# Kernel tuning notes

Hardware: AMD Instinct MI355X
Metric: run time of the kernel (lower is better)

The kernel has to match this reference:

```python
import jax, jax.numpy as jnp
import numpy as np

NUM_GROUPS = 32
EPS = 1e-6


def group_norm(x, scale, bias):
    # x: [b, c, l]
    b, c, l = x.shape
    xg = x.reshape(b, NUM_GROUPS, (c // NUM_GROUPS) * l)
    mean = jnp.mean(xg, axis=2, keepdims=True)
    var = jnp.var(xg, axis=2, keepdims=True)
    xn = ((xg - mean) * jax.lax.rsqrt(var + EPS)).reshape(b, c, l)
    return xn * scale[None, :, None] + bias[None, :, None]


def conv1x1(x, w, b):
    # pointwise conv: w [out_c, in_c], x [b, in_c, l]
    return jnp.einsum('oc,bcl->bol', w, x) + b[None, :, None]


def setup_inputs() -> dict:
    key = jax.random.key(0)
    ks = jax.random.split(key, 11)
    b, c, l = 4, 512, 4096
    s = 1.0 / np.sqrt(c)
    return {
        'x': jax.random.normal(ks[0], (b, c, l), jnp.float32),
        'gn_scale': jnp.ones((c,), jnp.float32),
        'gn_bias': jnp.zeros((c,), jnp.float32),
        'wq': jax.random.normal(ks[1], (c, c), jnp.float32) * s,
        'bq': jnp.zeros((c,), jnp.float32),
        'wk': jax.random.normal(ks[2], (c, c), jnp.float32) * s,
        'bk': jnp.zeros((c,), jnp.float32),
        'wv': jax.random.normal(ks[3], (c, c), jnp.float32) * s,
        'bv': jnp.zeros((c,), jnp.float32),
        'wp': jax.random.normal(ks[4], (c, c), jnp.float32) * s,
        'bp': jnp.zeros((c,), jnp.float32),
    }


def reference(x, gn_scale, gn_bias, wq, bq, wk, bk, wv, bv, wp, bp):
    h_ = group_norm(x, gn_scale, gn_bias)
    q = conv1x1(h_, wq, bq)  # [b, c, l]
    k = conv1x1(h_, wk, bk)
    v = conv1x1(h_, wv, bv)
    c = q.shape[1]
    # scores w[b,i,j] = sum_c q[b,c,i] k[b,c,j] * c^-0.5, softmax over j
    w = jnp.einsum('bci,bcj->bij', q, k) * (c ** -0.5)
    w = jax.nn.softmax(w, axis=2)
    # out[b,c,i] = sum_j w[b,i,j] v[b,c,j]
    h_ = jnp.einsum('bij,bcj->bci', w, v)
    h_ = conv1x1(h_, wp, bp)
    return x + h_
```

## Files before the change

kernel.cpp:

```cpp
#include <hip/hip_runtime.h>
#include <math.h>

#define BB 4
#define CC 512
#define LL 4096
#define NG 32
#define CPG 16
#define EPSV 1e-6f

typedef short s16x8 __attribute__((ext_vector_type(8)));
typedef __bf16 bf8v __attribute__((ext_vector_type(8)));
typedef float f32x4 __attribute__((ext_vector_type(4)));
typedef float f32x16 __attribute__((ext_vector_type(16)));
typedef int i32x4 __attribute__((ext_vector_type(4)));
typedef int i32x8 __attribute__((ext_vector_type(8)));
typedef unsigned short u16;
typedef unsigned char u8;

typedef const __attribute__((address_space(1))) void g1_void;
typedef __attribute__((address_space(3))) void l3_void;

#define ASM_SBAR() asm volatile("s_barrier" ::: "memory")
#define ASM_WAITV(N) asm volatile("s_waitcnt vmcnt(" #N ")" ::: "memory")

static __device__ __forceinline__ float bf2f(u16 h) {
    unsigned int u = ((unsigned int)h) << 16;
    union { unsigned int u; float f; } c; c.u = u; return c.f;
}
static __device__ __forceinline__ u16 f2bf(float f) {
    union { float f; unsigned int u; } c; c.f = f;
    unsigned int lsb = (c.u >> 16) & 1u;
    c.u += 0x7fffu + lsb;
    return (u16)(c.u >> 16);
}
static __device__ __forceinline__ u8 f2fp8(float f) {
    int v = __builtin_amdgcn_cvt_pk_fp8_f32(f, f, 0, false);
    return (u8)(v & 0xff);
}
static __device__ __forceinline__ bf8v ld_bf8(const u16* p) {
    return *reinterpret_cast<const bf8v*>(p);
}
static __device__ __forceinline__ i32x8 ld32(const u8* plo, const u8* phi) {
    i32x4 lo = *reinterpret_cast<const i32x4*>(plo);
    i32x4 hi = *reinterpret_cast<const i32x4*>(phi);
    return __builtin_shufflevector(lo, hi, 0, 1, 2, 3, 4, 5, 6, 7);
}
#define MFMA_SC(a, b, c) \
    __builtin_amdgcn_mfma_scale_f32_32x32x64_f8f6f4(a, b, c, 0, 0, 0, 0x7f, 0, 0x7f)

static __device__ __forceinline__ void gload16(const u16* g, u16* l) {
    __builtin_amdgcn_global_load_lds((g1_void*)g, (l3_void*)l, 16, 0, 0);
}
static __device__ __forceinline__ void gload16b(const u8* g, u8* l) {
    __builtin_amdgcn_global_load_lds((g1_void*)g, (l3_void*)l, 16, 0, 0);
}

__global__ __launch_bounds__(256) void wconv_kernel(const float* __restrict__ w0,
                                                    const float* __restrict__ w1,
                                                    const float* __restrict__ w2,
                                                    const float* __restrict__ w3,
                                                    u16* __restrict__ wbf) {
    int i = blockIdx.x * 256 + threadIdx.x;
    int wsel = blockIdx.y;
    const float* src = (wsel == 0) ? w0 : (wsel == 1) ? w1 : (wsel == 2) ? w2 : w3;
    float4 v = reinterpret_cast<const float4*>(src)[i];
    ushort4 o;
    o.x = f2bf(v.x); o.y = f2bf(v.y); o.z = f2bf(v.z); o.w = f2bf(v.w);
    reinterpret_cast<ushort4*>(wbf + (size_t)wsel * CC * CC)[i] = o;
}

__global__ __launch_bounds__(256) void biascat_kernel(const float* __restrict__ bq,
                                                      const float* __restrict__ bk,
                                                      const float* __restrict__ bv,
                                                      float* __restrict__ bcat,
                                                      float* __restrict__ rowsum) {
    int i = blockIdx.x * 256 + threadIdx.x;
    if (i < 3 * CC) {
        float v = (i < CC) ? bq[i] : (i < 2 * CC ? bk[i - CC] : bv[i - 2 * CC]);
        bcat[i] = v;
    }
    if (i < BB * LL) rowsum[i] = 0.f;
}

__global__ __launch_bounds__(256) void gn_stats_kernel(const float* __restrict__ x,
                                                       float2* __restrict__ stats) {
    int g = blockIdx.x, b = blockIdx.y, t = threadIdx.x;
    const float4* xp = reinterpret_cast<const float4*>(x + ((size_t)b * CC + (size_t)g * CPG) * LL);
    float s = 0.f, ss = 0.f;
    for (int it = 0; it < 64; ++it) {
        float4 v = xp[it * 256 + t];
        s += v.x + v.y + v.z + v.w;
        ss += v.x * v.x + v.y * v.y + v.z * v.z + v.w * v.w;
    }
    #pragma unroll
    for (int off = 32; off; off >>= 1) { s += __shfl_xor(s, off, 64); ss += __shfl_xor(ss, off, 64); }
    __shared__ float rs[4], rss[4];
    int wave = t >> 6, lane = t & 63;
    if (lane == 0) { rs[wave] = s; rss[wave] = ss; }
    __syncthreads();
    if (t == 0) {
        float S = rs[0] + rs[1] + rs[2] + rs[3];
        float SS = rss[0] + rss[1] + rss[2] + rss[3];
        float mean = S * (1.f / 65536.f);
        float var = SS * (1.f / 65536.f) - mean * mean;
        var = fmaxf(var, 0.f);
        stats[b * NG + g] = make_float2(mean, rsqrtf(var + EPSV));
    }
}

__global__ __launch_bounds__(256) void gn_norm_t_kernel(const float* __restrict__ x,
                                                        const float2* __restrict__ stats,
                                                        const float* __restrict__ gsc,
                                                        const float* __restrict__ gbi,
                                                        u16* __restrict__ hT) {
    int lt = blockIdx.x, ct = blockIdx.y, b = blockIdx.z;
    __shared__ u16 tile[64][72];
    int t = threadIdx.x;
    int cl0 = t >> 4, c4 = (t & 15) * 4;
    #pragma unroll
    for (int p = 0; p < 4; ++p) {
        int cl = p * 16 + cl0;
        int cg = ct * 64 + cl;
        float2 st = stats[b * NG + (cg >> 4)];
        float sc = gsc[cg] * st.y;
        float bi = gbi[cg];
        float4 v = *reinterpret_cast<const float4*>(x + ((size_t)b * CC + cg) * LL + lt * 64 + c4);
        tile[cl][c4 + 0] = f2bf((v.x - st.x) * sc + bi);
        tile[cl][c4 + 1] = f2bf((v.y - st.x) * sc + bi);
        tile[cl][c4 + 2] = f2bf((v.z - st.x) * sc + bi);
        tile[cl][c4 + 3] = f2bf((v.w - st.x) * sc + bi);
    }
    __syncthreads();
    int r = t >> 3, c8 = (t & 7) * 8;
    #pragma unroll
    for (int p = 0; p < 2; ++p) {
        int ll = p * 32 + r;
        s16x8 ov;
        #pragma unroll
        for (int j = 0; j < 8; ++j) ov[j] = (short)tile[c8 + j][ll];
        u16* hp = hT + ((size_t)b * LL + lt * 64 + ll) * CC + ct * 64 + c8;
        *reinterpret_cast<s16x8*>(hp) = ov;
    }
}

template <int MODE>
__global__ __launch_bounds__(256) void gemm_kernel(const u16* __restrict__ A, size_t asb, int lda,
                                                   const u16* __restrict__ B, size_t bsb, int ldb,
                                                   const float* __restrict__ bias,
                                                   u8* __restrict__ Oq, u8* __restrict__ Ok,
                                                   u8* __restrict__ Ov, size_t osb,
                                                   const float* __restrict__ xres,
                                                   float* __restrict__ fout, int K) {
    __shared__ u16 pool[24576];
    u8* pool8 = (u8*)pool;
    int mt = blockIdx.x, nt = blockIdx.y, b = blockIdx.z;
    int t = threadIdx.x;
    int wave = t >> 6, lane = t & 63;
    int wm = (wave >> 1) * 64, wn = (wave & 1) * 64;
    int l15 = lane & 15, quad = lane >> 4;
    f32x4 acc[4][4] = {};
    const u16* Ab = A + (size_t)b * asb + (size_t)mt * 128 * lda;
    const u16* Bb = B + (size_t)b * bsb + (size_t)nt * 128 * ldb;
    int swzg = ((lane & 3) ^ ((lane >> 2) & 3) ^ ((lane >> 4) & 3)) * 8;
    int row0 = wave * 16 + (lane >> 2);
    int row1 = 64 + row0;
    const u16* Ap0 = Ab + (size_t)row0 * lda + swzg;
    const u16* Ap1 = Ab + (size_t)row1 * lda + swzg;
    const u16* Bp0 = Bb + (size_t)row0 * ldb + swzg;
    const u16* Bp1 = Bb + (size_t)row1 * ldb + swzg;
    int wo = wave * 512;
    int swzf = (l15 & 3) ^ (l15 >> 2);
    int aoff = (wm + l15) * 32 + ((quad ^ swzf) * 8);
    int boff = (wn + l15) * 32 + ((quad ^ swzf) * 8);
    const int iters = K >> 5;
    gload16(Ap0, pool + wo);                gload16(Ap1, pool + 2048 + wo);
    gload16(Bp0, pool + 12288 + wo);        gload16(Bp1, pool + 12288 + 2048 + wo);
    gload16(Ap0 + 32, pool + 4096 + wo);    gload16(Ap1 + 32, pool + 4096 + 2048 + wo);
    gload16(Bp0 + 32, pool + 16384 + wo);   gload16(Bp1 + 32, pool + 16384 + 2048 + wo);
    int bs = 0;
    for (int i = 0; i < iters; ++i) {
        if (i + 1 < iters) { ASM_WAITV(4); } else { ASM_WAITV(0); }
        ASM_SBAR();
        const u16* As = pool + bs;
        const u16* Bs = pool + 12288 + bs;
        bf8v af[4], bfr[4];
        #pragma unroll
        for (int ii = 0; ii < 4; ++ii)
            af[ii] = ld_bf8(&As[aoff + ii * 512]);
        #pragma unroll
        for (int j = 0; j < 4; ++j)
            bfr[j] = ld_bf8(&Bs[boff + j * 512]);
        if (i + 2 < iters) {
            int kk = (i + 2) * 32;
            int nb = bs + 8192; if (nb >= 12288) nb -= 12288;
            u16* as = pool + nb; u16* bsp = pool + 12288 + nb;
            gload16(Ap0 + kk, as + wo);        gload16(Ap1 + kk, as + 2048 + wo);
            gload16(Bp0 + kk, bsp + wo);       gload16(Bp1 + kk, bsp + 2048 + wo);
        }
        __builtin_amdgcn_s_setprio(1);
        #pragma unroll
        for (int ii = 0; ii < 4; ++ii)
            #pragma unroll
            for (int j = 0; j < 4; ++j)
                acc[ii][j] = __builtin_amdgcn_mfma_f32_16x16x32_bf16(af[ii], bfr[j], acc[ii][j], 0, 0, 0);
        __builtin_amdgcn_s_setprio(0);
        bs += 4096; if (bs >= 12288) bs -= 12288;
    }
    if (MODE == 0) {
        int nt_sel = nt >> 2, ntl = nt & 3;
        if (nt_sel == 2) {
            __syncthreads();
            #pragma unroll
            for (int j = 0; j < 4; ++j) {
                float bv = bias[nt * 128 + wn + j * 16 + l15];
                #pragma unroll
                for (int i = 0; i < 4; ++i) {
                    int col = wn + j * 16 + l15;
                    int row = wm + i * 16 + quad * 4;
                    unsigned int w = __builtin_amdgcn_cvt_pk_fp8_f32(acc[i][j][0] + bv, acc[i][j][1] + bv, 0, false);
                    w = __builtin_amdgcn_cvt_pk_fp8_f32(acc[i][j][2] + bv, acc[i][j][3] + bv, w, true);
                    *reinterpret_cast<unsigned int*>(&pool8[col * 144 + row]) = w;
                }
            }
            __syncthreads();
            u8* Ob = Ov + (size_t)b * osb + (size_t)(ntl * 128) * LL + mt * 128;
            #pragma unroll
            for (int it = 0; it < 4; ++it) {
                int idx = it * 256 + t;
                int row = idx >> 3, ch = (idx & 7) * 16;
                *reinterpret_cast<float4*>(Ob + (size_t)row * LL + ch) =
                    *reinterpret_cast<const float4*>(&pool8[row * 144 + ch]);
            }
        } else {
            u8* Oc = (nt_sel == 0 ? Oq : Ok) + (size_t)b * osb
                     + (size_t)(mt * 128) * CC + ntl * 128 + wn + l15;
            #pragma unroll
            for (int j = 0; j < 4; ++j) {
                float bv = bias[nt * 128 + wn + j * 16 + l15];
                #pragma unroll
                for (int i = 0; i < 4; ++i)
                    #pragma unroll
                    for (int r = 0; r < 4; ++r) {
                        int row = wm + i * 16 + quad * 4 + r;
                        Oc[(size_t)row * CC + j * 16] = f2fp8(acc[i][j][r] + bv);
                    }
            }
        }
    } else {
        __syncthreads();
        #pragma unroll
        for (int j = 0; j < 4; ++j) {
            float bv = bias[nt * 128 + wn + j * 16 + l15];
            #pragma unroll
            for (int i = 0; i < 4; ++i)
                #pragma unroll
                for (int r = 0; r < 4; ++r) {
                    int row = wm + i * 16 + quad * 4 + r;
                    int col = wn + j * 16 + l15;
                    pool[col * 136 + row] = f2bf(acc[i][j][r] + bv);
                }
        }
        __syncthreads();
        const float* xb = xres + ((size_t)b * CC + nt * 128) * LL + mt * 128;
        float* ob = fout + ((size_t)b * CC + nt * 128) * LL + mt * 128;
        #pragma unroll
        for (int it = 0; it < 16; ++it) {
            int idx = it * 256 + t;
            int cl = idx >> 5, ch = (idx & 31) * 4;
            short4 pv = *reinterpret_cast<const short4*>(&pool[cl * 136 + ch]);
            float4 xv = *reinterpret_cast<const float4*>(xb + (size_t)cl * LL + ch);
            float4 ov;
            ov.x = xv.x + bf2f((u16)pv.x);
            ov.y = xv.y + bf2f((u16)pv.y);
            ov.z = xv.z + bf2f((u16)pv.z);
            ov.w = xv.w + bf2f((u16)pv.w);
            *reinterpret_cast<float4*>(ob + (size_t)cl * LL + ch) = ov;
        }
    }
}

template <int MODE>
__global__ __launch_bounds__(256) void gemm8_kernel(const u8* __restrict__ A, size_t asb, int lda,
                                                    const u8* __restrict__ B, size_t bsb, int ldb,
                                                    float scale,
                                                    u8* __restrict__ Out8, u16* __restrict__ OutH,
                                                    size_t osb, int Nout, int K,
                                                    float* __restrict__ rsum) {
    __shared__ u8 pool8[49152];
    int mt = blockIdx.x, nt = blockIdx.y, b = blockIdx.z;
    int t = threadIdx.x;
    int wave = t >> 6, lane = t & 63;
    int wm = (wave >> 1) * 64, wn = (wave & 1) * 64;
    int l15 = lane & 15, quad = lane >> 4;
    int l31 = lane & 31, hsel = lane >> 5;
    f32x4 acc16[4][4] = {};
    f32x16 accm[2][2] = {};
    int R = wave * 32 + (lane >> 1);
    int c16 = ((lane & 1) ^ (R & 1) ^ ((R >> 2) & 1)) * 16;
    const u8* Ap = A + (size_t)b * asb + (size_t)(mt * 128 + R) * lda + c16;
    const u8* Bp = B + (size_t)b * bsb + (size_t)(nt * 128 + R) * ldb + c16;
    int wo = wave * 1024;
    int p = (l15 & 1) ^ ((l15 >> 2) & 1);
    int fo = (((quad >> 1) ^ p) * 16) + (quad & 1) * 8;
    int abase = (wm + l15) * 32 + fo;
    int bbase = (wn + l15) * 32 + fo;
    int ra = wm + l31;
    int rb = wn + l31;
    int sa = (ra & 1) ^ ((ra >> 2) & 1);
    int sb = (rb & 1) ^ ((rb >> 2) & 1);
    int a_lo = hsel * 4096 + ra * 32 + sa * 16;
    int a_hi = hsel * 4096 + ra * 32 + 16 - sa * 16;
    int b_lo = hsel * 4096 + rb * 32 + sb * 16;
    int b_hi = hsel * 4096 + rb * 32 + 16 - sb * 16;
    const int iters = K >> 6;
    #define STG(ii, bsv) do { size_t kk = (size_t)(ii) * 64;               \
        gload16b(Ap + kk,      pool8 + (bsv) + wo);                        \
        gload16b(Ap + kk + 32, pool8 + (bsv) + 4096 + wo);                 \
        gload16b(Bp + kk,      pool8 + 24576 + (bsv) + wo);                \
        gload16b(Bp + kk + 32, pool8 + 24576 + (bsv) + 4096 + wo); } while (0)
    STG(0, 0);
    STG(1, 8192);
    int bs = 0;
    for (int i = 0; i < iters; ++i) {
        if (i + 1 < iters) { ASM_WAITV(4); } else { ASM_WAITV(0); }
        ASM_SBAR();
        const u8* As = pool8 + bs;
        const u8* Bs = pool8 + 24576 + bs;
        if (MODE == 1) {
            long af0[4], bf0[4], af1[4], bf1[4];
            #pragma unroll
            for (int ii = 0; ii < 4; ++ii) {
                af0[ii] = *reinterpret_cast<const long*>(As + abase + ii * 512);
                af1[ii] = *reinterpret_cast<const long*>(As + 4096 + abase + ii * 512);
            }
            #pragma unroll
            for (int j = 0; j < 4; ++j) {
                bf0[j] = *reinterpret_cast<const long*>(Bs + bbase + j * 512);
                bf1[j] = *reinterpret_cast<const long*>(Bs + 4096 + bbase + j * 512);
            }
            if (i + 2 < iters) {
                int nb = bs + 16384; if (nb >= 24576) nb -= 24576;
                STG(i + 2, nb);
            }
            __builtin_amdgcn_s_setprio(1);
            #pragma unroll
            for (int ii = 0; ii < 4; ++ii)
                #pragma unroll
                for (int j = 0; j < 4; ++j)
                    acc16[ii][j] = __builtin_amdgcn_mfma_f32_16x16x32_fp8_fp8(af0[ii], bf0[j], acc16[ii][j], 0, 0, 0);
            #pragma unroll
            for (int ii = 0; ii < 4; ++ii)
                #pragma unroll
                for (int j = 0; j < 4; ++j)
                    acc16[ii][j] = __builtin_amdgcn_mfma_f32_16x16x32_fp8_fp8(af1[ii], bf1[j], acc16[ii][j], 0, 0, 0);
            __builtin_amdgcn_s_setprio(0);
        } else {
            i32x8 a0 = ld32(As + a_lo, As + a_hi);
            i32x8 a1 = ld32(As + 1024 + a_lo, As + 1024 + a_hi);
            i32x8 b0 = ld32(Bs + b_lo, Bs + b_hi);
            i32x8 b1 = ld32(Bs + 1024 + b_lo, Bs + 1024 + b_hi);
            if (i + 2 < iters) {
                int nb = bs + 16384; if (nb >= 24576) nb -= 24576;
                STG(i + 2, nb);
            }
            __builtin_amdgcn_s_setprio(1);
            accm[0][0] = MFMA_SC(a0, b0, accm[0][0]);
            accm[0][1] = MFMA_SC(a0, b1, accm[0][1]);
            accm[1][0] = MFMA_SC(a1, b0, accm[1][0]);
            accm[1][1] = MFMA_SC(a1, b1, accm[1][1]);
            __builtin_amdgcn_s_setprio(0);
        }
        bs += 8192; if (bs >= 24576) bs -= 24576;
    }
    #undef STG
    if (MODE == 1) {
        u8* Ob = Out8 + (size_t)b * osb + (size_t)(mt * 128) * Nout + nt * 128 + wn + l15;
        #pragma unroll
        for (int i = 0; i < 4; ++i) {
            #pragma unroll
            for (int r = 0; r < 4; ++r) {
                int row = wm + i * 16 + quad * 4 + r;
                u8* rp = Ob + (size_t)row * Nout;
                float part = 0.f;
                #pragma unroll
                for (int j = 0; j < 4; ++j) {
                    float v = __expf(acc16[i][j][r] * scale - 3.0f);
                    part += v;
                    rp[j * 16] = f2fp8(v);
                }
                part += __shfl_xor(part, 1, 64);
                part += __shfl_xor(part, 2, 64);
                part += __shfl_xor(part, 4, 64);
                part += __shfl_xor(part, 8, 64);
                if (l15 == 0)
                    atomicAdd(rsum + (size_t)b * LL + mt * 128 + row, part);
            }
        }
    } else {
        __syncthreads();
        u16* poolh = (u16*)pool8;
        const float* rbase2 = rsum + (size_t)b * LL + mt * 128;
        #pragma unroll
        for (int i = 0; i < 2; ++i)
            #pragma unroll
            for (int rg = 0; rg < 4; ++rg) {
                int row0 = wm + i * 32 + 8 * rg + 4 * hsel;
                float4 rv = *reinterpret_cast<const float4*>(rbase2 + row0);
                float iv[4] = {1.f / rv.x, 1.f / rv.y, 1.f / rv.z, 1.f / rv.w};
                #pragma unroll
                for (int rr = 0; rr < 4; ++rr) {
                    int reg = rg * 4 + rr;
                    int row = row0 + rr;
                    poolh[row * 136 + wn + l31]      = f2bf(accm[i][0][reg] * iv[rr]);
                    poolh[row * 136 + wn + 32 + l31] = f2bf(accm[i][1][reg] * iv[rr]);
                }
            }
        __syncthreads();
        u16* Ob = OutH + (size_t)b * osb + (size_t)(mt * 128) * Nout + nt * 128;
        #pragma unroll
        for (int it = 0; it < 8; ++it) {
            int idx = it * 256 + t;
            int row = idx >> 4, ch = (idx & 15) * 8;
            s16x8 val = *reinterpret_cast<const s16x8*>(&poolh[row * 136 + ch]);
            *reinterpret_cast<s16x8*>(Ob + (size_t)row * Nout + ch) = val;
        }
    }
}

extern "C" void kernel_launch(void* const* d_in, const int* in_sizes, int n_in,
                              void* d_out, int out_size, void* d_ws, size_t ws_size,
                              hipStream_t stream) {
    const float* x   = (const float*)d_in[0];
    const float* gsc = (const float*)d_in[1];
    const float* gbi = (const float*)d_in[2];
    const float* wq  = (const float*)d_in[3];
    const float* bq  = (const float*)d_in[4];
    const float* wk  = (const float*)d_in[5];
    const float* bk  = (const float*)d_in[6];
    const float* wv  = (const float*)d_in[7];
    const float* bv  = (const float*)d_in[8];
    const float* wp  = (const float*)d_in[9];
    const float* bp  = (const float*)d_in[10];
    float* out = (float*)d_out;

    char* ws = (char*)d_ws;
    const size_t SZ   = (size_t)BB * LL * CC * 2;
    const size_t QSZ  = (size_t)BB * LL * CC;
    const size_t WQSZ = (size_t)4 * CC * CC * 2;
    const size_t RSZ  = (size_t)BB * LL * 4;
    u16* bufA = (u16*)(ws);
    u8*  q8   = (u8*)(ws + SZ);
    u8*  k8   = (u8*)(ws + SZ + QSZ);
    u8*  v8   = (u8*)(ws + SZ + 2 * QSZ);
    u16* wbf  = (u16*)(ws + SZ + 3 * QSZ);
    float2* stats = (float2*)(ws + SZ + 3 * QSZ + WQSZ);
    float* bcat   = (float*)(ws + SZ + 3 * QSZ + WQSZ + 4096);
    float* rowsum = (float*)(ws + SZ + 3 * QSZ + WQSZ + 4096 + 8192);
    u8* S8 = (u8*)(ws + SZ + 3 * QSZ + WQSZ + 4096 + 8192 + RSZ);
    const float scale = 0.044194173824159216f;
    const size_t BLC = (size_t)LL * CC;

    wconv_kernel<<<dim3(256, 4), 256, 0, stream>>>(wq, wk, wv, wp, wbf);
    biascat_kernel<<<dim3(64), 256, 0, stream>>>(bq, bk, bv, bcat, rowsum);
    gn_stats_kernel<<<dim3(NG, BB), 256, 0, stream>>>(x, stats);
    gn_norm_t_kernel<<<dim3(64, 8, BB), 256, 0, stream>>>(x, stats, gsc, gbi, bufA);
    gemm_kernel<0><<<dim3(32, 12, BB), 256, 0, stream>>>(bufA, BLC, CC, wbf, 0, CC, bcat,
                                                         q8, k8, v8, BLC, nullptr, nullptr, CC);
    gemm8_kernel<1><<<dim3(32, 32, BB), 256, 0, stream>>>(q8, BLC, CC, k8, BLC, CC, scale,
                                                          S8, nullptr, (size_t)LL * LL, LL, CC, rowsum);
    gemm8_kernel<2><<<dim3(32, 4, BB), 256, 0, stream>>>(S8, (size_t)LL * LL, LL, v8, BLC, LL, 1.f,
                                                         nullptr, bufA, BLC, CC, LL, rowsum);
    gemm_kernel<3><<<dim3(32, 4, BB), 256, 0, stream>>>(bufA, BLC, CC, wbf + 3 * CC * CC, 0, CC,
                                                        bp, nullptr, nullptr, nullptr, 0, x, out, CC);
}
```

Before: 299.9 us.

## Split MODE 1 fp8 score GEMM into 4-stage, 32-wide K pipeline

Separates the MODE 1 (QK^T score) path from the MODE 2 path. MODE 1 now loads a 32-element K slice per iteration into a 4-deep ring of LDS buffers, keeping three stages in flight instead of two 64-wide stages. Its LDS footprint drops to 32 KB, which may allow more resident blocks per CU, and the deeper prefetch aims to hide global load latency. The trade-off is twice as many barriers and loop iterations, with fewer MFMAs between each sync.

```diff
diff --git a/kernel.cpp b/kernel.cpp
--- a/kernel.cpp
+++ b/kernel.cpp
@@ -286,7 +286,7 @@
                                                     u8* __restrict__ Out8, u16* __restrict__ OutH,
                                                     size_t osb, int Nout, int K,
                                                     float* __restrict__ rsum) {
-    __shared__ u8 pool8[49152];
+    __shared__ u8 pool8[MODE == 1 ? 32768 : 49152];
     int mt = blockIdx.x, nt = blockIdx.y, b = blockIdx.z;
     int t = threadIdx.x;
     int wave = t >> 6, lane = t & 63;
@@ -312,68 +312,37 @@
     int a_hi = hsel * 4096 + ra * 32 + 16 - sa * 16;
     int b_lo = hsel * 4096 + rb * 32 + sb * 16;
     int b_hi = hsel * 4096 + rb * 32 + 16 - sb * 16;
-    const int iters = K >> 6;
-    #define STG(ii, bsv) do { size_t kk = (size_t)(ii) * 64;               \
-        gload16b(Ap + kk,      pool8 + (bsv) + wo);                        \
-        gload16b(Ap + kk + 32, pool8 + (bsv) + 4096 + wo);                 \
-        gload16b(Bp + kk,      pool8 + 24576 + (bsv) + wo);                \
-        gload16b(Bp + kk + 32, pool8 + 24576 + (bsv) + 4096 + wo); } while (0)
-    STG(0, 0);
-    STG(1, 8192);
-    int bs = 0;
-    for (int i = 0; i < iters; ++i) {
-        if (i + 1 < iters) { ASM_WAITV(4); } else { ASM_WAITV(0); }
-        ASM_SBAR();
-        const u8* As = pool8 + bs;
-        const u8* Bs = pool8 + 24576 + bs;
-        if (MODE == 1) {
-            long af0[4], bf0[4], af1[4], bf1[4];
-            #pragma unroll
-            for (int ii = 0; ii < 4; ++ii) {
-                af0[ii] = *reinterpret_cast<const long*>(As + abase + ii * 512);
-                af1[ii] = *reinterpret_cast<const long*>(As + 4096 + abase + ii * 512);
-            }
-            #pragma unroll
-            for (int j = 0; j < 4; ++j) {
-                bf0[j] = *reinterpret_cast<const long*>(Bs + bbase + j * 512);
-                bf1[j] = *reinterpret_cast<const long*>(Bs + 4096 + bbase + j * 512);
-            }
-            if (i + 2 < iters) {
-                int nb = bs + 16384; if (nb >= 24576) nb -= 24576;
-                STG(i + 2, nb);
-            }
+    if (MODE == 1) {
+        const int iters = K >> 5;
+        #define STG1(ii) do { size_t kk = (size_t)(ii) * 32; int bb = ((ii) & 3) * 4096; \
+            gload16b(Ap + kk, pool8 + bb + wo);                                          \
+            gload16b(Bp + kk, pool8 + 16384 + bb + wo); } while (0)
+        STG1(0); STG1(1); STG1(2);
+        for (int i = 0; i < iters; ++i) {
+            if (i + 2 < iters) { ASM_WAITV(4); }
+            else if (i + 1 < iters) { ASM_WAITV(2); }
+            else { ASM_WAITV(0); }
+            ASM_SBAR();
+            int bb = (i & 3) * 4096;
+            const u8* As = pool8 + bb;
+            const u8* Bs = pool8 + 16384 + bb;
+            long af[4], bf[4];
+            #pragma unroll
+            for (int ii = 0; ii < 4; ++ii)
+                af[ii] = *reinterpret_cast<const long*>(As + abase + ii * 512);
+            #pragma unroll
+            for (int j = 0; j < 4; ++j)
+                bf[j] = *reinterpret_cast<const long*>(Bs + bbase + j * 512);
+            if (i + 3 < iters) STG1(i + 3);
             __builtin_amdgcn_s_setprio(1);
             #pragma unroll
             for (int ii = 0; ii < 4; ++ii)
                 #pragma unroll
                 for (int j = 0; j < 4; ++j)
-                    acc16[ii][j] = __builtin_amdgcn_mfma_f32_16x16x32_fp8_fp8(af0[ii], bf0[j], acc16[ii][j], 0, 0, 0);
-            #pragma unroll
-            for (int ii = 0; ii < 4; ++ii)
-                #pragma unroll
-                for (int j = 0; j < 4; ++j)
-                    acc16[ii][j] = __builtin_amdgcn_mfma_f32_16x16x32_fp8_fp8(af1[ii], bf1[j], acc16[ii][j], 0, 0, 0);
+                    acc16[ii][j] = __builtin_amdgcn_mfma_f32_16x16x32_fp8_fp8(af[ii], bf[j], acc16[ii][j], 0, 0, 0);
             __builtin_amdgcn_s_setprio(0);
-        } else {
-            i32x8 a0 = ld32(As + a_lo, As + a_hi);
-            i32x8 a1 = ld32(As + 1024 + a_lo, As + 1024 + a_hi);
-            i32x8 b0 = ld32(Bs + b_lo, Bs + b_hi);
-            i32x8 b1 = ld32(Bs + 1024 + b_lo, Bs + 1024 + b_hi);
-            if (i + 2 < iters) {
-                int nb = bs + 16384; if (nb >= 24576) nb -= 24576;
-                STG(i + 2, nb);
-            }
-            __builtin_amdgcn_s_setprio(1);
-            accm[0][0] = MFMA_SC(a0, b0, accm[0][0]);
-            accm[0][1] = MFMA_SC(a0, b1, accm[0][1]);
-            accm[1][0] = MFMA_SC(a1, b0, accm[1][0]);
-            accm[1][1] = MFMA_SC(a1, b1, accm[1][1]);
-            __builtin_amdgcn_s_setprio(0);
-        }
-        bs += 8192; if (bs >= 24576) bs -= 24576;
-    }
-    #undef STG
-    if (MODE == 1) {
+        }
+        #undef STG1
         u8* Ob = Out8 + (size_t)b * osb + (size_t)(mt * 128) * Nout + nt * 128 + wn + l15;
         #pragma unroll
         for (int i = 0; i < 4; ++i) {
@@ -397,6 +366,37 @@
             }
         }
     } else {
+        const int iters = K >> 6;
+        #define STG2(ii, bsv) do { size_t kk = (size_t)(ii) * 64;              \
+            gload16b(Ap + kk,      pool8 + (bsv) + wo);                        \
+            gload16b(Ap + kk + 32, pool8 + (bsv) + 4096 + wo);                 \
+            gload16b(Bp + kk,      pool8 + 24576 + (bsv) + wo);                \
+            gload16b(Bp + kk + 32, pool8 + 24576 + (bsv) + 4096 + wo); } while (0)
+        STG2(0, 0);
+        STG2(1, 8192);
+        int bs = 0;
+        for (int i = 0; i < iters; ++i) {
+            if (i + 1 < iters) { ASM_WAITV(4); } else { ASM_WAITV(0); }
+            ASM_SBAR();
+            const u8* As = pool8 + bs;
+            const u8* Bs = pool8 + 24576 + bs;
+            i32x8 a0 = ld32(As + a_lo, As + a_hi);
+            i32x8 a1 = ld32(As + 1024 + a_lo, As + 1024 + a_hi);
+            i32x8 b0 = ld32(Bs + b_lo, Bs + b_hi);
+            i32x8 b1 = ld32(Bs + 1024 + b_lo, Bs + 1024 + b_hi);
+            if (i + 2 < iters) {
+                int nb = bs + 16384; if (nb >= 24576) nb -= 24576;
+                STG2(i + 2, nb);
+            }
+            __builtin_amdgcn_s_setprio(1);
+            accm[0][0] = MFMA_SC(a0, b0, accm[0][0]);
+            accm[0][1] = MFMA_SC(a0, b1, accm[0][1]);
+            accm[1][0] = MFMA_SC(a1, b0, accm[1][0]);
+            accm[1][1] = MFMA_SC(a1, b1, accm[1][1]);
+            __builtin_amdgcn_s_setprio(0);
+            bs += 8192; if (bs >= 24576) bs -= 24576;
+        }
+        #undef STG2
         __syncthreads();
         u16* poolh = (u16*)pool8;
         const float* rbase2 = rsum + (size_t)b * LL + mt * 128;
```

After: 311.6 us. 1.04x slower.

## Halve PV GEMM M-tile to 64 rows and fold bias setup into weight conversion

Applied to the files above, without the earlier changes.

The attention-times-V GEMM (MODE 2) now uses 64-row M tiles instead of 128, doubling its grid from 512 to 1024 blocks. Each wave computes a 32x64 output with two scaled fp8 MFMAs per K step, and the LDS footprint for that mode shrinks. The aim is to fill the 256 CUs better, since the old grid left many idle during a long K=4096 reduction. The trade is that each V tile is loaded twice as often. Separately, the bias concat and rowsum zeroing move into the weight-conversion kernel, removing one launch.

```diff
diff --git a/kernel.cpp b/kernel.cpp
--- a/kernel.cpp
+++ b/kernel.cpp
@@ -59,7 +59,12 @@
                                                     const float* __restrict__ w1,
                                                     const float* __restrict__ w2,
                                                     const float* __restrict__ w3,
-                                                    u16* __restrict__ wbf) {
+                                                    u16* __restrict__ wbf,
+                                                    const float* __restrict__ bq,
+                                                    const float* __restrict__ bk,
+                                                    const float* __restrict__ bv,
+                                                    float* __restrict__ bcat,
+                                                    float* __restrict__ rowsum) {
     int i = blockIdx.x * 256 + threadIdx.x;
     int wsel = blockIdx.y;
     const float* src = (wsel == 0) ? w0 : (wsel == 1) ? w1 : (wsel == 2) ? w2 : w3;
@@ -67,19 +72,11 @@
     ushort4 o;
     o.x = f2bf(v.x); o.y = f2bf(v.y); o.z = f2bf(v.z); o.w = f2bf(v.w);
     reinterpret_cast<ushort4*>(wbf + (size_t)wsel * CC * CC)[i] = o;
-}
-
-__global__ __launch_bounds__(256) void biascat_kernel(const float* __restrict__ bq,
-                                                      const float* __restrict__ bk,
-                                                      const float* __restrict__ bv,
-                                                      float* __restrict__ bcat,
-                                                      float* __restrict__ rowsum) {
-    int i = blockIdx.x * 256 + threadIdx.x;
-    if (i < 3 * CC) {
-        float v = (i < CC) ? bq[i] : (i < 2 * CC ? bk[i - CC] : bv[i - 2 * CC]);
-        bcat[i] = v;
-    }
-    if (i < BB * LL) rowsum[i] = 0.f;
+    if (wsel == 0) {
+        if (i < 3 * CC)
+            bcat[i] = (i < CC) ? bq[i] : (i < 2 * CC ? bk[i - CC] : bv[i - 2 * CC]);
+        if (i < BB * LL) rowsum[i] = 0.f;
+    }
 }
 
 __global__ __launch_bounds__(256) void gn_stats_kernel(const float* __restrict__ x,
@@ -286,47 +283,38 @@
                                                     u8* __restrict__ Out8, u16* __restrict__ OutH,
                                                     size_t osb, int Nout, int K,
                                                     float* __restrict__ rsum) {
-    __shared__ u8 pool8[49152];
+    __shared__ u8 pool8[MODE == 1 ? 49152 : 36864];
     int mt = blockIdx.x, nt = blockIdx.y, b = blockIdx.z;
     int t = threadIdx.x;
     int wave = t >> 6, lane = t & 63;
-    int wm = (wave >> 1) * 64, wn = (wave & 1) * 64;
     int l15 = lane & 15, quad = lane >> 4;
     int l31 = lane & 31, hsel = lane >> 5;
-    f32x4 acc16[4][4] = {};
-    f32x16 accm[2][2] = {};
     int R = wave * 32 + (lane >> 1);
     int c16 = ((lane & 1) ^ (R & 1) ^ ((R >> 2) & 1)) * 16;
-    const u8* Ap = A + (size_t)b * asb + (size_t)(mt * 128 + R) * lda + c16;
-    const u8* Bp = B + (size_t)b * bsb + (size_t)(nt * 128 + R) * ldb + c16;
     int wo = wave * 1024;
-    int p = (l15 & 1) ^ ((l15 >> 2) & 1);
-    int fo = (((quad >> 1) ^ p) * 16) + (quad & 1) * 8;
-    int abase = (wm + l15) * 32 + fo;
-    int bbase = (wn + l15) * 32 + fo;
-    int ra = wm + l31;
-    int rb = wn + l31;
-    int sa = (ra & 1) ^ ((ra >> 2) & 1);
-    int sb = (rb & 1) ^ ((rb >> 2) & 1);
-    int a_lo = hsel * 4096 + ra * 32 + sa * 16;
-    int a_hi = hsel * 4096 + ra * 32 + 16 - sa * 16;
-    int b_lo = hsel * 4096 + rb * 32 + sb * 16;
-    int b_hi = hsel * 4096 + rb * 32 + 16 - sb * 16;
-    const int iters = K >> 6;
-    #define STG(ii, bsv) do { size_t kk = (size_t)(ii) * 64;               \
-        gload16b(Ap + kk,      pool8 + (bsv) + wo);                        \
-        gload16b(Ap + kk + 32, pool8 + (bsv) + 4096 + wo);                 \
-        gload16b(Bp + kk,      pool8 + 24576 + (bsv) + wo);                \
-        gload16b(Bp + kk + 32, pool8 + 24576 + (bsv) + 4096 + wo); } while (0)
-    STG(0, 0);
-    STG(1, 8192);
-    int bs = 0;
-    for (int i = 0; i < iters; ++i) {
-        if (i + 1 < iters) { ASM_WAITV(4); } else { ASM_WAITV(0); }
-        ASM_SBAR();
-        const u8* As = pool8 + bs;
-        const u8* Bs = pool8 + 24576 + bs;
-        if (MODE == 1) {
+    if (MODE == 1) {
+        int wm = (wave >> 1) * 64, wn = (wave & 1) * 64;
+        f32x4 acc16[4][4] = {};
+        const u8* Ap = A + (size_t)b * asb + (size_t)(mt * 128 + R) * lda + c16;
+        const u8* Bp = B + (size_t)b * bsb + (size_t)(nt * 128 + R) * ldb + c16;
+        int p = (l15 & 1) ^ ((l15 >> 2) & 1);
+        int fo = (((quad >> 1) ^ p) * 16) + (quad & 1) * 8;
+        int abase = (wm + l15) * 32 + fo;
+        int bbase = (wn + l15) * 32 + fo;
+        const int iters = K >> 6;
+        #define STG1(ii, bsv) do { size_t kk = (size_t)(ii) * 64;              \
+            gload16b(Ap + kk,      pool8 + (bsv) + wo);                        \
+            gload16b(Ap + kk + 32, pool8 + (bsv) + 4096 + wo);                 \
+            gload16b(Bp + kk,      pool8 + 24576 + (bsv) + wo);                \
+            gload16b(Bp + kk + 32, pool8 + 24576 + (bsv) + 4096 + wo); } while (0)
+        STG1(0, 0);
+        STG1(1, 8192);
+        int bs = 0;
+        for (int i = 0; i < iters; ++i) {
+            if (i + 1 < iters) { ASM_WAITV(4); } else { ASM_WAITV(0); }
+            ASM_SBAR();
+            const u8* As = pool8 + bs;
+            const u8* Bs = pool8 + 24576 + bs;
             long af0[4], bf0[4], af1[4], bf1[4];
             #pragma unroll
             for (int ii = 0; ii < 4; ++ii) {
@@ -340,7 +328,7 @@
             }
             if (i + 2 < iters) {
                 int nb = bs + 16384; if (nb >= 24576) nb -= 24576;
-                STG(i + 2, nb);
+                STG1(i + 2, nb);
             }
             __builtin_amdgcn_s_setprio(1);
             #pragma unroll
@@ -354,26 +342,9 @@
                 for (int j = 0; j < 4; ++j)
                     acc16[ii][j] = __builtin_amdgcn_mfma_f32_16x16x32_fp8_fp8(af1[ii], bf1[j], acc16[ii][j], 0, 0, 0);
             __builtin_amdgcn_s_setprio(0);
-        } else {
-            i32x8 a0 = ld32(As + a_lo, As + a_hi);
-            i32x8 a1 = ld32(As + 1024 + a_lo, As + 1024 + a_hi);
-            i32x8 b0 = ld32(Bs + b_lo, Bs + b_hi);
-            i32x8 b1 = ld32(Bs + 1024 + b_lo, Bs + 1024 + b_hi);
-            if (i + 2 < iters) {
-                int nb = bs + 16384; if (nb >= 24576) nb -= 24576;
-                STG(i + 2, nb);
-            }
-            __builtin_amdgcn_s_setprio(1);
-            accm[0][0] = MFMA_SC(a0, b0, accm[0][0]);
-            accm[0][1] = MFMA_SC(a0, b1, accm[0][1]);
-            accm[1][0] = MFMA_SC(a1, b0, accm[1][0]);
-            accm[1][1] = MFMA_SC(a1, b1, accm[1][1]);
-            __builtin_amdgcn_s_setprio(0);
-        }
-        bs += 8192; if (bs >= 24576) bs -= 24576;
-    }
-    #undef STG
-    if (MODE == 1) {
+            bs += 8192; if (bs >= 24576) bs -= 24576;
+        }
+        #undef STG1
         u8* Ob = Out8 + (size_t)b * osb + (size_t)(mt * 128) * Nout + nt * 128 + wn + l15;
         #pragma unroll
         for (int i = 0; i < 4; ++i) {
@@ -397,28 +368,69 @@
             }
         }
     } else {
+        int wm2 = (wave >> 1) * 32, wn2 = (wave & 1) * 64;
+        f32x16 accm[2] = {};
+        int rA = (t >> 1) & 63, hA = t >> 7, eA = t & 1;
+        int gA = eA ^ (rA & 1) ^ ((rA >> 2) & 1);
+        const u8* ApA = A + (size_t)b * asb + (size_t)(mt * 64 + rA) * lda + hA * 32 + gA * 16;
+        const u8* BpB = B + (size_t)b * bsb + (size_t)(nt * 128 + R) * ldb + c16;
+        int ra = wm2 + l31;
+        int rb = wn2 + l31;
+        int sa = (ra & 1) ^ ((ra >> 2) & 1);
+        int sb = (rb & 1) ^ ((rb >> 2) & 1);
+        int a_lo = hsel * 2048 + ra * 32 + sa * 16;
+        int a_hi = hsel * 2048 + ra * 32 + 16 - sa * 16;
+        int b_lo = hsel * 4096 + rb * 32 + sb * 16;
+        int b_hi = hsel * 4096 + rb * 32 + 16 - sb * 16;
+        const int iters = K >> 6;
+        #define STG2(ii, ba_, bb_) do { size_t kk = (size_t)(ii) * 64;         \
+            gload16b(ApA + kk,      pool8 + (ba_) + wo);                       \
+            gload16b(BpB + kk,      pool8 + 12288 + (bb_) + wo);               \
+            gload16b(BpB + kk + 32, pool8 + 12288 + (bb_) + 4096 + wo); } while (0)
+        STG2(0, 0, 0);
+        STG2(1, 4096, 8192);
+        int ba = 0, bb = 0;
+        for (int i = 0; i < iters; ++i) {
+            if (i + 1 < iters) { ASM_WAITV(3); } else { ASM_WAITV(0); }
+            ASM_SBAR();
+            const u8* As = pool8 + ba;
+            const u8* Bs = pool8 + 12288 + bb;
+            i32x8 a0 = ld32(As + a_lo, As + a_hi);
+            i32x8 b0 = ld32(Bs + b_lo, Bs + b_hi);
+            i32x8 b1 = ld32(Bs + 1024 + b_lo, Bs + 1024 + b_hi);
+            if (i + 2 < iters) {
+                int na = ba + 8192; if (na >= 12288) na -= 12288;
+                int nb = bb + 16384; if (nb >= 24576) nb -= 24576;
+                STG2(i + 2, na, nb);
+            }
+            __builtin_amdgcn_s_setprio(1);
+            accm[0] = MFMA_SC(a0, b0, accm[0]);
+            accm[1] = MFMA_SC(a0, b1, accm[1]);
+            __builtin_amdgcn_s_setprio(0);
+            ba += 4096; if (ba >= 12288) ba -= 12288;
+            bb += 8192; if (bb >= 24576) bb -= 24576;
+        }
+        #undef STG2
         __syncthreads();
         u16* poolh = (u16*)pool8;
-        const float* rbase2 = rsum + (size_t)b * LL + mt * 128;
-        #pragma unroll
-        for (int i = 0; i < 2; ++i)
-            #pragma unroll
-            for (int rg = 0; rg < 4; ++rg) {
-                int row0 = wm + i * 32 + 8 * rg + 4 * hsel;
-                float4 rv = *reinterpret_cast<const float4*>(rbase2 + row0);
-                float iv[4] = {1.f / rv.x, 1.f / rv.y, 1.f / rv.z, 1.f / rv.w};
-                #pragma unroll
-                for (int rr = 0; rr < 4; ++rr) {
-                    int reg = rg * 4 + rr;
-                    int row = row0 + rr;
-                    poolh[row * 136 + wn + l31]      = f2bf(accm[i][0][reg] * iv[rr]);
-                    poolh[row * 136 + wn + 32 + l31] = f2bf(accm[i][1][reg] * iv[rr]);
-                }
-            }
+        const float* rbase2 = rsum + (size_t)b * LL + mt * 64;
+        #pragma unroll
+        for (int rg = 0; rg < 4; ++rg) {
+            int row0 = wm2 + 8 * rg + 4 * hsel;
+            float4 rv = *reinterpret_cast<const float4*>(rbase2 + row0);
+            float iv[4] = {1.f / rv.x, 1.f / rv.y, 1.f / rv.z, 1.f / rv.w};
+            #pragma unroll
+            for (int rr = 0; rr < 4; ++rr) {
+                int reg = rg * 4 + rr;
+                int row = row0 + rr;
+                poolh[row * 136 + wn2 + l31]      = f2bf(accm[0][reg] * iv[rr]);
+                poolh[row * 136 + wn2 + 32 + l31] = f2bf(accm[1][reg] * iv[rr]);
+            }
+        }
         __syncthreads();
-        u16* Ob = OutH + (size_t)b * osb + (size_t)(mt * 128) * Nout + nt * 128;
-        #pragma unroll
-        for (int it = 0; it < 8; ++it) {
+        u16* Ob = OutH + (size_t)b * osb + (size_t)(mt * 64) * Nout + nt * 128;
+        #pragma unroll
+        for (int it = 0; it < 4; ++it) {
             int idx = it * 256 + t;
             int row = idx >> 4, ch = (idx & 15) * 8;
             s16x8 val = *reinterpret_cast<const s16x8*>(&poolh[row * 136 + ch]);
@@ -460,15 +472,15 @@
     const float scale = 0.044194173824159216f;
     const size_t BLC = (size_t)LL * CC;
 
-    wconv_kernel<<<dim3(256, 4), 256, 0, stream>>>(wq, wk, wv, wp, wbf);
-    biascat_kernel<<<dim3(64), 256, 0, stream>>>(bq, bk, bv, bcat, rowsum);
+    wconv_kernel<<<dim3(256, 4), 256, 0, stream>>>(wq, wk, wv, wp, wbf,
+                                                   bq, bk, bv, bcat, rowsum);
     gn_stats_kernel<<<dim3(NG, BB), 256, 0, stream>>>(x, stats);
     gn_norm_t_kernel<<<dim3(64, 8, BB), 256, 0, stream>>>(x, stats, gsc, gbi, bufA);
     gemm_kernel<0><<<dim3(32, 12, BB), 256, 0, stream>>>(bufA, BLC, CC, wbf, 0, CC, bcat,
                                                          q8, k8, v8, BLC, nullptr, nullptr, CC);
     gemm8_kernel<1><<<dim3(32, 32, BB), 256, 0, stream>>>(q8, BLC, CC, k8, BLC, CC, scale,
                                                           S8, nullptr, (size_t)LL * LL, LL, CC, rowsum);
-    gemm8_kernel<2><<<dim3(32, 4, BB), 256, 0, stream>>>(S8, (size_t)LL * LL, LL, v8, BLC, LL, 1.f,
+    gemm8_kernel<2><<<dim3(64, 4, BB), 256, 0, stream>>>(S8, (size_t)LL * LL, LL, v8, BLC, LL, 1.f,
                                                          nullptr, bufA, BLC, CC, LL, rowsum);
     gemm_kernel<3><<<dim3(32, 4, BB), 256, 0, stream>>>(bufA, BLC, CC, wbf + 3 * CC * CC, 0, CC,
                                                         bp, nullptr, nullptr, nullptr, 0, x, out, CC);
```

Measured after the change: 317.1 us. +5.7%, slower.
